# Kernel optimization log

Measured on AMD Instinct MI355X. Metric: run time of the kernel, lower is better.

## Reference

```python
import jax, jax.numpy as jnp
import numpy as np

NUM_EMBEDDINGS = 4096
EMBEDDING_DIM = 64
COMMITMENT_LOSS_FACTOR = 0.25


def setup_inputs() -> dict:
    key = jax.random.key(0)
    k1, k2 = jax.random.split(key)
    z = jax.random.normal(k1, (16, 64, 64, EMBEDDING_DIM), dtype=jnp.float32)
    init_range = 1.0 / NUM_EMBEDDINGS
    embeddings = jax.random.uniform(
        k2, (NUM_EMBEDDINGS, EMBEDDING_DIM), dtype=jnp.float32,
        minval=-init_range, maxval=init_range)
    return {"z": z, "embeddings": embeddings}


def reference(z, embeddings):
    # z: [B, H, W, D] channels-last latents; embeddings: [K, D] codebook
    B, H, W, D = z.shape
    z_flat = z.reshape(-1, D)  # [N, D]
    # Squared Euclidean distances (argmin-equivalent to cdist p=2, sqrt is monotone)
    d2 = (jnp.sum(z_flat * z_flat, axis=1, keepdims=True)
          - 2.0 * (z_flat @ embeddings.T)
          + jnp.sum(embeddings * embeddings, axis=1))  # [N, K]
    closest = jnp.argmin(d2, axis=1)  # [N]
    quantized = embeddings[closest].reshape(z.shape)  # gather == one_hot @ embeddings
    quantized_indices = closest.reshape(B, H, W)
    # eval-mode forward (no EMA buffer update)
    commitment_loss = jnp.sum((jax.lax.stop_gradient(quantized) - z) ** 2)
    loss = COMMITMENT_LOSS_FACTOR * commitment_loss
    quantized = z + jax.lax.stop_gradient(quantized - z)  # straight-through
    return (quantized.transpose(0, 3, 1, 2),      # [B, D, H, W]
            quantized_indices[:, None, :, :],      # [B, 1, H, W]
            loss)
```

## Files before the change

### kernel.cpp

```cpp
#include <hip/hip_runtime.h>


typedef _Float16 half8 __attribute__((ext_vector_type(8)));
typedef float f32x4 __attribute__((ext_vector_type(4)));

#define NCODES 4096
#define DIM 64
#define NROWS 65536
#define OUT_IDX_OFF 4194304
#define OUT_LOSS_OFF 4259840

#define WS_EHI   0u
#define WS_EE    524288u
#define WS_RLOSS 540672u
#define WS_TU1   802816u
#define WS_TK1   1327104u
#define WS_TU2   1851392u
#define WS_TK23  2375680u
#define WS_TU3   2899968u
#define WS_TU4   3424256u
#define WS_LISTB 3948544u
#define WS_CNTB  4210688u
#define WS_PART  4210944u

__device__ __forceinline__ float pairwise_sumsq64(const float* v) {
    float r[8];
#pragma unroll
    for (int j = 0; j < 8; ++j) r[j] = __fmul_rn(v[j], v[j]);
#pragma unroll
    for (int m = 1; m < 8; ++m) {
#pragma unroll
        for (int j = 0; j < 8; ++j)
            r[j] = __fadd_rn(r[j], __fmul_rn(v[8 * m + j], v[8 * m + j]));
    }
    float s01 = __fadd_rn(r[0], r[1]);
    float s23 = __fadd_rn(r[2], r[3]);
    float s45 = __fadd_rn(r[4], r[5]);
    float s67 = __fadd_rn(r[6], r[7]);
    return __fadd_rn(__fadd_rn(s01, s23), __fadd_rn(s45, s67));
}

__device__ __forceinline__ float exact_d2(const float* __restrict__ emb, int k,
                                          const float* zr, float zz, float eev) {
    const float4* ep = reinterpret_cast<const float4*>(emb + (size_t)k * DIM);
    float da = 0.f;
#pragma unroll
    for (int q = 0; q < 16; ++q) {
        float4 A = ep[q];
        da += A.x * zr[4 * q + 0]; da += A.y * zr[4 * q + 1];
        da += A.z * zr[4 * q + 2]; da += A.w * zr[4 * q + 3];
    }
    return __fadd_rn(__fsub_rn(zz, __fmul_rn(2.0f, da)), eev);
}

__device__ __forceinline__ void gload_lds16(const void* g, void* l) {
    __builtin_amdgcn_global_load_lds(
        (const __attribute__((address_space(1))) unsigned int*)g,
        (__attribute__((address_space(3))) unsigned int*)l, 16, 0, 0);
}

#define WAITVM(n)                                               \
    {                                                           \
        asm volatile("s_waitcnt vmcnt(" #n ")" ::: "memory");   \
        __builtin_amdgcn_sched_barrier(0);                      \
    }

__global__ void vq_prep(const float* __restrict__ emb, _Float16* __restrict__ ehi,
                        float* __restrict__ ee) {
    int k = blockIdx.x * 256 + threadIdx.x;
    float v[DIM];
    const float4* p = reinterpret_cast<const float4*>(emb + (size_t)k * DIM);
#pragma unroll
    for (int i = 0; i < 16; ++i) {
        float4 a = p[i];
        v[4 * i + 0] = a.x; v[4 * i + 1] = a.y; v[4 * i + 2] = a.z; v[4 * i + 3] = a.w;
    }
    ee[k] = pairwise_sumsq64(v);
#pragma unroll
    for (int i = 0; i < 8; ++i) {
        half8 h;
#pragma unroll
        for (int j = 0; j < 8; ++j) h[j] = (_Float16)(v[8 * i + j] * 256.0f);
        *reinterpret_cast<half8*>(ehi + (size_t)k * DIM + 8 * i) = h;
    }
}

#define INS4MAX(x, xid, s)                                    \
    {                                                         \
        bool q1 = (x) > M1[s], q2 = (x) > M2[s], q3 = (x) > M3[s]; \
        M4[s] = q3 ? M3[s] : fmaxf((x), M4[s]);               \
        M3[s] = q2 ? M2[s] : (q3 ? (x) : M3[s]);              \
        G3[s] = q2 ? G2[s] : (q3 ? (xid) : G3[s]);            \
        M2[s] = q1 ? M1[s] : (q2 ? (x) : M2[s]);              \
        G2[s] = q1 ? G1[s] : (q2 ? (xid) : G2[s]);            \
        M1[s] = q1 ? (x) : M1[s];                             \
        G1[s] = q1 ? (xid) : G1[s];                           \
    }

__launch_bounds__(256, 4)
__global__ void vq_scan(const float* __restrict__ z, const _Float16* __restrict__ ehi,
                        float* __restrict__ tU1, int* __restrict__ tK1,
                        float* __restrict__ tU2, int* __restrict__ tK23,
                        float* __restrict__ tU3, float* __restrict__ tU4) {
    __shared__ float4 sB[4][512];

    const int tid = threadIdx.x;
    const int lane = tid & 63;
    const int w = tid >> 6;
    const int rlo = lane & 15;
    const int quad = lane >> 4;
    const int half = blockIdx.y;
    const int rowbase = blockIdx.x * 128 + w * 32;

    half8 zhi[2][2];
#pragma unroll
    for (int rt = 0; rt < 2; ++rt) {
        const float* zp = z + (size_t)(rowbase + rt * 16 + rlo) * DIM + quad * 8;
#pragma unroll
        for (int ks = 0; ks < 2; ++ks) {
            float4 a = *reinterpret_cast<const float4*>(zp + ks * 32);
            float4 b = *reinterpret_cast<const float4*>(zp + ks * 32 + 4);
            float f[8] = {a.x, a.y, a.z, a.w, b.x, b.y, b.z, b.w};
            half8 hi;
#pragma unroll
            for (int e = 0; e < 8; ++e) hi[e] = (_Float16)f[e];
            zhi[rt][ks] = hi;
        }
    }

    int gOff[2];
#pragma unroll
    for (int i = 0; i < 2; ++i) {
        int L = tid + i * 256;
        int T = L >> 6, u = L & 63;
        int code = (T >> 1) * 16 + (u & 15);
        int dg = (T & 1) * 4 + (u >> 4);
        gOff[i] = (code * 8 + dg) * 16;
    }
    const char* srcHiB = (const char*)ehi + (size_t)half * 2048 * 128;

    auto issue = [&](int cc, int bb) {
        const char* hs = srcHiB + (size_t)cc * 8192;
        char* dH = (char*)&sB[bb][0];
#pragma unroll
        for (int i = 0; i < 2; ++i)
            gload_lds16(hs + gOff[i], dH + (tid + i * 256) * 16);
    };

    issue(0, 0);
    issue(1, 1);

    float M1[2], M2[2], M3[2], M4[2];
    int G1[2], G2[2], G3[2];
#pragma unroll
    for (int s = 0; s < 2; ++s) {
        M1[s] = -3e38f; M2[s] = -3e38f; M3[s] = -3e38f; M4[s] = -3e38f;
        G1[s] = 0; G2[s] = 0; G3[s] = 0;
    }
    const f32x4 zero4 = {0.f, 0.f, 0.f, 0.f};

#pragma unroll 1
    for (int c = 0; c < 32; ++c) {
        if (c < 30) {
            issue(c + 2, (c + 2) & 3);
            WAITVM(4);
        } else if (c == 30) {
            WAITVM(2);
        } else {
            WAITVM(0);
        }
        __builtin_amdgcn_s_barrier();
        __builtin_amdgcn_sched_barrier(0);

        const float4* bh = sB[c & 3];
        float run[2];
#pragma unroll
        for (int s = 0; s < 2; ++s) run[s] = -3e38f;
#pragma unroll
        for (int t = 0; t < 4; ++t) {
            half8 a0h = __builtin_bit_cast(half8, bh[(t * 2 + 0) * 64 + lane]);
            half8 a1h = __builtin_bit_cast(half8, bh[(t * 2 + 1) * 64 + lane]);
#pragma unroll
            for (int rt = 0; rt < 2; ++rt) {
                f32x4 acc = __builtin_amdgcn_mfma_f32_16x16x32_f16(a0h, zhi[rt][0], zero4, 0, 0, 0);
                acc = __builtin_amdgcn_mfma_f32_16x16x32_f16(a1h, zhi[rt][1], acc, 0, 0, 0);
                run[rt] = fmaxf(run[rt],
                                fmaxf(fmaxf(acc[0], acc[1]), fmaxf(acc[2], acc[3])));
            }
        }
        const int gb = (c << 6) + (quad << 2);
#pragma unroll
        for (int s = 0; s < 2; ++s) INS4MAX(run[s], gb, s);
        __builtin_amdgcn_sched_barrier(0);
    }

#pragma unroll
    for (int s = 0; s < 2; ++s) {
#pragma unroll
        for (int d = 16; d < 64; d <<= 1) {
            float o1 = __shfl_xor(M1[s], d); int p1 = __shfl_xor(G1[s], d);
            float o2 = __shfl_xor(M2[s], d); int p2 = __shfl_xor(G2[s], d);
            float o3 = __shfl_xor(M3[s], d); int p3 = __shfl_xor(G3[s], d);
            float o4 = __shfl_xor(M4[s], d);
            INS4MAX(o1, p1, s);
            INS4MAX(o2, p2, s);
            INS4MAX(o3, p3, s);
            M4[s] = fmaxf(M4[s], o4);
        }
    }

    if (lane < 16) {
        const int hoff = half << 11;
#pragma unroll
        for (int s = 0; s < 2; ++s) {
            int grow = rowbase + s * 16 + lane;
            size_t idx = (size_t)half * NROWS + grow;
            tU1[idx] = M1[s] * -0.0078125f;
            tU2[idx] = M2[s] * -0.0078125f;
            tU3[idx] = M3[s] * -0.0078125f;
            tU4[idx] = M4[s] * -0.0078125f;
            tK1[idx] = G1[s] + hoff;
            tK23[idx] = (G2[s] + hoff) | ((G3[s] + hoff) << 16);
        }
    }
}

__global__ void vq_finish(const float* __restrict__ z, const float* __restrict__ emb,
                          const float* __restrict__ ee,
                          const float* __restrict__ tU1, const int* __restrict__ tK1,
                          const float* __restrict__ tU2, const int* __restrict__ tK23,
                          const float* __restrict__ tU3, const float* __restrict__ tU4,
                          float* __restrict__ out,
                          int* __restrict__ listB, int* __restrict__ cntB) {
    const int row = blockIdx.x * 256 + threadIdx.x;

    float u1 = tU1[row]; int g1 = tK1[row];
    float u2 = tU2[row];
    float u3 = tU3[row]; float u4 = tU4[row];
    int k23 = tK23[row];
    int g2 = k23 & 0xFFFF, g3 = ((unsigned)k23) >> 16;
    {
        float b1 = tU1[NROWS + row]; int h1 = tK1[NROWS + row];
        float b2 = tU2[NROWS + row];
        float b3 = tU3[NROWS + row]; float b4 = tU4[NROWS + row];
        int hk = tK23[NROWS + row];
        int h2 = hk & 0xFFFF, h3 = ((unsigned)hk) >> 16;
#define INSU(bv, bi)                                           \
        { bool q1 = (bv) < u1, q2 = (bv) < u2, q3 = (bv) < u3; \
          u4 = q3 ? u3 : fminf((bv), u4);                      \
          u3 = q2 ? u2 : (q3 ? (bv) : u3);                     \
          g3 = q2 ? g2 : (q3 ? (bi) : g3);                     \
          u2 = q1 ? u1 : (q2 ? (bv) : u2);                     \
          g2 = q1 ? g1 : (q2 ? (bi) : g2);                     \
          u1 = q1 ? (bv) : u1;                                 \
          g1 = q1 ? (bi) : g1; }
        INSU(b1, h1);
        INSU(b2, h2);
        INSU(b3, h3);
        u4 = fminf(u4, b4);
#undef INSU
    }

    float zr[DIM];
    {
        const float4* zp = reinterpret_cast<const float4*>(z + (size_t)row * DIM);
#pragma unroll
        for (int i = 0; i < 16; ++i) {
            float4 a = zp[i];
            zr[4 * i + 0] = a.x; zr[4 * i + 1] = a.y; zr[4 * i + 2] = a.z; zr[4 * i + 3] = a.w;
        }
    }
    float zzs = 0.f;
#pragma unroll
    for (int i = 0; i < DIM; ++i) zzs = fmaf(zr[i], zr[i], zzs);

    float delta = ((zzs > 120.f) ? 3.4e-5f : 1.7e-5f) + 2.5e-5f;

    if (u4 - u1 < delta) {
        int p = atomicAdd(cntB, 1);
        listB[p] = row;
    }

    const float zz = pairwise_sumsq64(zr);
    float best = 3e38f; int kb = 0x7fffffff;
    int secs[3]; int nsec = 1; secs[0] = g1;
    if (u2 - u1 < delta) {
        secs[1] = g2; nsec = 2;
        if (u3 - u1 < delta) { secs[2] = g3; nsec = 3; }
    }
    for (int si = 0; si < nsec; ++si) {
        const int base = secs[si];
#pragma unroll
        for (int t = 0; t < 4; ++t) {
#pragma unroll
            for (int j = 0; j < 4; ++j) {
                int k = base + t * 16 + j;
                float d2 = exact_d2(emb, k, zr, zz, ee[k]);
                if (d2 < best || (d2 == best && k < kb)) { best = d2; kb = k; }
            }
        }
    }
    out[OUT_IDX_OFF + row] = (float)kb;
}

__launch_bounds__(256, 4)
__global__ void vq_emit(const float* __restrict__ z, const float* __restrict__ emb,
                        float* __restrict__ out, float* __restrict__ rowloss,
                        double* __restrict__ part) {
    __shared__ float zs[64 * 65];
    __shared__ float qs[64 * 65];
    __shared__ float ls[64 * 5];
    const int tid = threadIdx.x;
    const int rl = tid >> 2;
    const int j = tid & 3;
    const int row = blockIdx.x * 64 + rl;

    {
        const float4* zp = reinterpret_cast<const float4*>(
            z + (size_t)blockIdx.x * 4096 + (size_t)tid * 16);
        float4 a = zp[0], b = zp[1], c = zp[2], d = zp[3];
        float v[16] = {a.x, a.y, a.z, a.w, b.x, b.y, b.z, b.w,
                       c.x, c.y, c.z, c.w, d.x, d.y, d.z, d.w};
        float* dst = &zs[rl * 65 + j * 16];
#pragma unroll
        for (int i = 0; i < 16; ++i) dst[i] = v[i];
    }
    {
        const int kb = (int)out[OUT_IDX_OFF + row];
        const float4* qp = reinterpret_cast<const float4*>(
            emb + (size_t)kb * DIM + j * 16);
        float4 a = qp[0], b = qp[1], c = qp[2], d = qp[3];
        float v[16] = {a.x, a.y, a.z, a.w, b.x, b.y, b.z, b.w,
                       c.x, c.y, c.z, c.w, d.x, d.y, d.z, d.w};
        float* dst = &qs[rl * 65 + j * 16];
#pragma unroll
        for (int i = 0; i < 16; ++i) dst[i] = v[i];
    }
    __syncthreads();

    const int hw_l = tid & 63;
    const int w = tid >> 6;
    const int bimg = row >> 12;
    const int hwb = (blockIdx.x * 64) & 4095;
    float* ob = out + (size_t)bimg * 262144 + hwb + hw_l;
    float lp = 0.f;
#pragma unroll
    for (int k = 0; k < 16; ++k) {
        const int d = w * 16 + k;
        float qv = qs[hw_l * 65 + d];
        float zv = zs[hw_l * 65 + d];
        float df = qv - zv;
        lp = fmaf(df, df, lp);
        ob[(size_t)d * 4096] = qv;
    }
    ls[hw_l * 5 + w] = lp;
    __syncthreads();

    if (tid < 64) {
        float r01 = ls[tid * 5 + 0] + ls[tid * 5 + 1];
        float r23 = ls[tid * 5 + 2] + ls[tid * 5 + 3];
        float rsum = r01 + r23;
        rowloss[blockIdx.x * 64 + tid] = rsum;
        double s = (double)rsum;
#pragma unroll
        for (int d = 1; d < 64; d <<= 1) s += __shfl_xor(s, d);
        if (tid == 0) atomicAdd(&part[blockIdx.x >> 2], s);
    }
}

__global__ void vq_fallback(const float* __restrict__ z, const float* __restrict__ emb,
                            const float* __restrict__ ee, const int* __restrict__ listB,
                            const int* __restrict__ cntB, float* __restrict__ out,
                            const float* __restrict__ rowloss, double* __restrict__ part) {
    __shared__ float sZ[DIM];
    __shared__ unsigned long long sK[4];
    __shared__ int sKb;
    const int n = *cntB;
    const int tid = threadIdx.x;
    const int lane = tid & 63;
    const int w = tid >> 6;

    for (int i = blockIdx.x; i < n; i += 1024) {
        const int row = listB[i];
        __syncthreads();
        if (tid < DIM) sZ[tid] = z[(size_t)row * DIM + tid];
        __syncthreads();
        float zr[DIM];
#pragma unroll
        for (int q = 0; q < DIM; ++q) zr[q] = sZ[q];
        const float zz = pairwise_sumsq64(zr);

        unsigned long long best = ~0ull;
#pragma unroll 1
        for (int j = 0; j < 16; ++j) {
            int c = tid + j * 256;
            float d2 = exact_d2(emb, c, zr, zz, ee[c]);
            unsigned long long key =
                (((unsigned long long)__float_as_uint(d2)) << 32) | (unsigned)c;
            best = key < best ? key : best;
        }
#pragma unroll
        for (int d = 1; d < 64; d <<= 1) {
            unsigned long long o2 = __shfl_xor(best, d);
            best = o2 < best ? o2 : best;
        }
        if (lane == 0) sK[w] = best;
        __syncthreads();
        if (tid == 0) {
            unsigned long long b = sK[0];
            b = sK[1] < b ? sK[1] : b;
            b = sK[2] < b ? sK[2] : b;
            b = sK[3] < b ? sK[3] : b;
            sKb = (int)(b & 0xFFFFFFFFu);
        }
        __syncthreads();
        const int kb = sKb;
        if (tid < DIM) {
            const float qv = emb[(size_t)kb * DIM + tid];
            const float zv = sZ[tid];
            int bimg = row >> 12, hw = row & 4095;
            out[(size_t)bimg * 262144 + (size_t)tid * 4096 + hw] = qv;
            float lp = (qv - zv) * (qv - zv);
#pragma unroll
            for (int d = 1; d < 64; d <<= 1) lp += __shfl_xor(lp, d);
            if (tid == 0) {
                double dl = (double)lp - (double)rowloss[row];
                atomicAdd(&part[row >> 8], dl);
                out[OUT_IDX_OFF + row] = (float)kb;
            }
        }
    }
}

__global__ void vq_red2(const double* __restrict__ part, float* __restrict__ out_loss) {
    __shared__ double sd[256];
    sd[threadIdx.x] = part[threadIdx.x];
    __syncthreads();
    for (int st = 128; st > 0; st >>= 1) {
        if (threadIdx.x < st) sd[threadIdx.x] += sd[threadIdx.x + st];
        __syncthreads();
    }
    if (threadIdx.x == 0) out_loss[0] = (float)(0.25 * sd[0]);
}

extern "C" void kernel_launch(void* const* d_in, const int* in_sizes, int n_in,
                              void* d_out, int out_size, void* d_ws, size_t ws_size,
                              hipStream_t stream) {
    const float* z = (const float*)d_in[0];
    const float* emb = (const float*)d_in[1];
    float* out = (float*)d_out;
    char* ws = (char*)d_ws;

    _Float16* ehi = (_Float16*)(ws + WS_EHI);
    float* ee = (float*)(ws + WS_EE);
    float* rowloss = (float*)(ws + WS_RLOSS);
    float* tU1 = (float*)(ws + WS_TU1);
    int*   tK1 = (int*)(ws + WS_TK1);
    float* tU2 = (float*)(ws + WS_TU2);
    int*   tK23 = (int*)(ws + WS_TK23);
    float* tU3 = (float*)(ws + WS_TU3);
    float* tU4 = (float*)(ws + WS_TU4);
    int* listB = (int*)(ws + WS_LISTB);
    int* cntB  = (int*)(ws + WS_CNTB);
    double* part = (double*)(ws + WS_PART);

    hipMemsetAsync(cntB, 0, sizeof(int), stream);
    hipMemsetAsync(part, 0, 256 * sizeof(double), stream);
    vq_prep<<<NCODES / 256, 256, 0, stream>>>(emb, ehi, ee);
    vq_scan<<<dim3(NROWS / 128, 2), 256, 0, stream>>>(z, ehi, tU1, tK1, tU2, tK23, tU3, tU4);
    vq_finish<<<NROWS / 256, 256, 0, stream>>>(z, emb, ee, tU1, tK1, tU2, tK23, tU3, tU4,
                                               out, listB, cntB);
    vq_emit<<<NROWS / 64, 256, 0, stream>>>(z, emb, out, rowloss, part);
    vq_fallback<<<1024, 256, 0, stream>>>(z, emb, ee, listB, cntB, out, rowloss, part);
    vq_red2<<<1, 256, 0, stream>>>(part, out + OUT_LOSS_OFF);
}
```

Baseline: 181.0 us.

## Split vq_finish rescoring across four threads per row with LDS-staged z

vq_finish now gives each row four threads instead of one. The z row is loaded coalesced into shared memory, and each thread rescores a quarter of the candidate codes. Per-thread (distance, index) results are packed into a 64-bit key and reduced across the four lanes with xor shuffles. The intent is to cut per-thread serial exact-distance work and the strided z loads, and to raise parallelism. The cost is four times the blocks, redundant reads of the top-4 tables, and a __syncthreads.

New measurement: 256.7 us. 41.9% more time.

```diff
diff --git a/kernel.cpp b/kernel.cpp
--- a/kernel.cpp
+++ b/kernel.cpp
@@ -225,6 +225,7 @@
     }
 }
 
+__launch_bounds__(256, 4)
 __global__ void vq_finish(const float* __restrict__ z, const float* __restrict__ emb,
                           const float* __restrict__ ee,
                           const float* __restrict__ tU1, const int* __restrict__ tK1,
@@ -232,7 +233,18 @@
                           const float* __restrict__ tU3, const float* __restrict__ tU4,
                           float* __restrict__ out,
                           int* __restrict__ listB, int* __restrict__ cntB) {
-    const int row = blockIdx.x * 256 + threadIdx.x;
+    __shared__ float zs[64][68];
+    const int tid = threadIdx.x;
+    const int rl = tid >> 2;
+    const int j = tid & 3;
+    const int row = blockIdx.x * 64 + rl;
+
+    {
+        const float4* zp = reinterpret_cast<const float4*>(z + (size_t)row * DIM + j * 16);
+        float4 c0 = zp[0], c1 = zp[1], c2 = zp[2], c3 = zp[3];
+        float4* dst = reinterpret_cast<float4*>(&zs[rl][j * 16]);
+        dst[0] = c0; dst[1] = c1; dst[2] = c2; dst[3] = c3;
+    }
 
     float u1 = tU1[row]; int g1 = tK1[row];
     float u2 = tU2[row];
@@ -261,9 +273,11 @@
 #undef INSU
     }
 
+    __syncthreads();
+
     float zr[DIM];
     {
-        const float4* zp = reinterpret_cast<const float4*>(z + (size_t)row * DIM);
+        const float4* zp = reinterpret_cast<const float4*>(&zs[rl][0]);
 #pragma unroll
         for (int i = 0; i < 16; ++i) {
             float4 a = zp[i];
@@ -276,13 +290,13 @@
 
     float delta = ((zzs > 120.f) ? 3.4e-5f : 1.7e-5f) + 2.5e-5f;
 
-    if (u4 - u1 < delta) {
+    if (j == 0 && u4 - u1 < delta) {
         int p = atomicAdd(cntB, 1);
         listB[p] = row;
     }
 
     const float zz = pairwise_sumsq64(zr);
-    float best = 3e38f; int kb = 0x7fffffff;
+    unsigned long long bestkey = ~0ull;
     int secs[3]; int nsec = 1; secs[0] = g1;
     if (u2 - u1 < delta) {
         secs[1] = g2; nsec = 2;
@@ -292,15 +306,20 @@
         const int base = secs[si];
 #pragma unroll
         for (int t = 0; t < 4; ++t) {
-#pragma unroll
-            for (int j = 0; j < 4; ++j) {
-                int k = base + t * 16 + j;
-                float d2 = exact_d2(emb, k, zr, zz, ee[k]);
-                if (d2 < best || (d2 == best && k < kb)) { best = d2; kb = k; }
-            }
-        }
-    }
-    out[OUT_IDX_OFF + row] = (float)kb;
+            int k = base + t * 16 + j;
+            float d2 = exact_d2(emb, k, zr, zz, ee[k]);
+            unsigned long long key =
+                (((unsigned long long)__float_as_uint(d2)) << 32) | (unsigned)k;
+            bestkey = key < bestkey ? key : bestkey;
+        }
+    }
+    {
+        unsigned long long o1 = __shfl_xor(bestkey, 1);
+        bestkey = o1 < bestkey ? o1 : bestkey;
+        unsigned long long o2 = __shfl_xor(bestkey, 2);
+        bestkey = o2 < bestkey ? o2 : bestkey;
+    }
+    if (j == 0) out[OUT_IDX_OFF + row] = (float)(int)(bestkey & 0xFFFFFFFFu);
 }
 
 __launch_bounds__(256, 4)
@@ -468,8 +487,8 @@
     hipMemsetAsync(part, 0, 256 * sizeof(double), stream);
     vq_prep<<<NCODES / 256, 256, 0, stream>>>(emb, ehi, ee);
     vq_scan<<<dim3(NROWS / 128, 2), 256, 0, stream>>>(z, ehi, tU1, tK1, tU2, tK23, tU3, tU4);
-    vq_finish<<<NROWS / 256, 256, 0, stream>>>(z, emb, ee, tU1, tK1, tU2, tK23, tU3, tU4,
-                                               out, listB, cntB);
+    vq_finish<<<NROWS / 64, 256, 0, stream>>>(z, emb, ee, tU1, tK1, tU2, tK23, tU3, tU4,
+                                              out, listB, cntB);
     vq_emit<<<NROWS / 64, 256, 0, stream>>>(z, emb, out, rowloss, part);
     vq_fallback<<<1024, 256, 0, stream>>>(z, emb, ee, listB, cntB, out, rowloss, part);
     vq_red2<<<1, 256, 0, stream>>>(part, out + OUT_LOSS_OFF);
```
